# Performance work log

Hardware: AMD Instinct MI355X
Metric: run time of the kernel (lower is better)

Reference implementation:

```python
import jax, jax.numpy as jnp
import numpy as np

L = 16            # number of levels
F = 2             # features per level
T = 1 << 17       # hashmap size per level (power of 2)
N_TREES = 8       # forest blocks
N = 2_000_000     # query points
RES = np.array([16, 22, 30, 41, 55, 75, 102, 139, 188, 256, 348, 472, 642, 872, 1184, 1608], dtype=np.int64)
# 8 trilinear corner offsets [8,3]
OFFS = np.stack(np.meshgrid([0, 1], [0, 1], [0, 1], indexing='ij'), axis=-1).reshape(8, 3).astype(np.int32)
PRIMES = (np.uint32(1), np.uint32(2654435761), np.uint32(805459861))


def _hash(coords):
    # coords: [N,8,3] int32 grid corner coords -> [N,8] table index (NGP spatial hash)
    c = coords.astype(jnp.uint32)
    h = (c[..., 0] * PRIMES[0]) ^ (c[..., 1] * PRIMES[1]) ^ (c[..., 2] * PRIMES[2])
    return (h & jnp.uint32(T - 1)).astype(jnp.int32)


def setup_inputs() -> dict:
    key = jax.random.key(0)
    k1, k2, k3 = jax.random.split(key, 3)
    block_x = jax.random.uniform(k1, (N, 3), minval=-1.0, maxval=1.0, dtype=jnp.float32)
    bound = 1e-4
    params = jax.random.uniform(k2, (N_TREES, L, T, F), minval=-bound, maxval=bound, dtype=jnp.float32)
    block_inds = jax.random.randint(k3, (N,), 0, N_TREES)
    return {"block_x": block_x, "params": params, "block_inds": block_inds}


def reference(block_x, params, block_inds):
    # block_x in [-1,1]^3 -> [0,1]^3 (matches `block_x / 2.0 + 0.5` in forward)
    x01 = block_x * 0.5 + 0.5
    offs = jnp.asarray(OFFS)                    # [8,3]
    offs_b = jnp.asarray(OFFS, dtype=bool)      # [8,3]
    outs = []
    for l in range(L):
        R = int(RES[l])
        pos = x01 * (R - 1)                     # [N,3]
        p0 = jnp.floor(pos)
        w = pos - p0                            # trilinear fracs [N,3]
        p0i = p0.astype(jnp.int32)
        corners = jnp.clip(p0i[:, None, :] + offs[None], 0, R - 1)   # [N,8,3]
        idx = _hash(corners)                                          # [N,8]
        feats = params[block_inds[:, None], l, idx, :]                # [N,8,F] per-tree gather
        wc = jnp.prod(jnp.where(offs_b[None], w[:, None, :], 1.0 - w[:, None, :]), axis=-1)  # [N,8]
        outs.append(jnp.einsum('nc,ncf->nf', wc, feats))              # [N,F]
    return jnp.concatenate(outs, axis=-1)        # [N, L*F]
```

## Files before the change

### kernel.cpp

```cpp
#include <hip/hip_runtime.h>

#define NLEVELS 16
#define TSIZE 131072
#define TMASK (TSIZE - 1)
#define NBUCK 32768

typedef float f32x4 __attribute__((ext_vector_type(4)));

__device__ __constant__ float RM1_TAB[16] = {
    15.f, 21.f, 29.f, 40.f, 54.f, 74.f, 101.f, 138.f,
    187.f, 255.f, 347.f, 471.f, 641.f, 871.f, 1183.f, 1607.f
};

__device__ __forceinline__ unsigned spread4(unsigned v) {
    v = (v | (v << 4)) & 0x0C3u;
    v = (v | (v << 2)) & 0x249u;
    return v;
}

__device__ __forceinline__ unsigned bucket_key(float x, float y, float z, unsigned tree) {
    const int cx = min(max((int)((x * 0.5f + 0.5f) * 16.f), 0), 15);
    const int cy = min(max((int)((y * 0.5f + 0.5f) * 16.f), 0), 15);
    const int cz = min(max((int)((z * 0.5f + 0.5f) * 16.f), 0), 15);
    const unsigned m = spread4((unsigned)cx) | (spread4((unsigned)cy) << 1)
                     | (spread4((unsigned)cz) << 2);
    return (tree << 12) | m;
}


__global__ __launch_bounds__(256) void k_hist(const float* __restrict__ xs,
                                              const int* __restrict__ inds, int N,
                                              unsigned* __restrict__ hist) {
    const int i = blockIdx.x * 256 + threadIdx.x;
    if (i >= N) return;
    const unsigned key = bucket_key(xs[3 * i], xs[3 * i + 1], xs[3 * i + 2],
                                    (unsigned)(inds[i] & 7));
    atomicAdd(&hist[key], 1u);
}

__global__ __launch_bounds__(1024) void k_scan(const unsigned* __restrict__ hist,
                                               unsigned* __restrict__ cursor) {
    __shared__ unsigned sums[1024];
    const int t = threadIdx.x;
    const int per = NBUCK / 1024;
    unsigned s = 0;
    #pragma unroll
    for (int j = 0; j < per; ++j) s += hist[t * per + j];
    sums[t] = s;
    __syncthreads();
    for (int off = 1; off < 1024; off <<= 1) {
        const unsigned add = (t >= off) ? sums[t - off] : 0u;
        __syncthreads();
        sums[t] += add;
        __syncthreads();
    }
    unsigned run = (t == 0) ? 0u : sums[t - 1];
    #pragma unroll
    for (int j = 0; j < per; ++j) {
        cursor[t * per + j] = run;
        run += hist[t * per + j];
    }
}

__global__ __launch_bounds__(256) void k_scatter(const float* __restrict__ xs,
                                                 const int* __restrict__ inds, int N,
                                                 unsigned* __restrict__ cursor,
                                                 float4* __restrict__ sorted) {
    const int i = blockIdx.x * 256 + threadIdx.x;
    if (i >= N) return;
    const float x = xs[3 * i], y = xs[3 * i + 1], z = xs[3 * i + 2];
    const unsigned tree = (unsigned)(inds[i] & 7);
    const unsigned key = bucket_key(x, y, z, tree);
    const unsigned pos = atomicAdd(&cursor[key], 1u);
    sorted[pos] = make_float4(x, y, z, __uint_as_float(((unsigned)i) | (tree << 24)));
}


__device__ __forceinline__ void level_load(const float4 p, int tree, int l,
                                           const float* __restrict__ params,
                                           float2 f[8],
                                           float& wx, float& wy, float& wz) {
    const float rm1 = RM1_TAB[l];
    const int rmax = (int)rm1;

    const float px = (p.x * 0.5f + 0.5f) * rm1;
    const float py = (p.y * 0.5f + 0.5f) * rm1;
    const float pz = (p.z * 0.5f + 0.5f) * rm1;
    const float fx = floorf(px), fy = floorf(py), fz = floorf(pz);
    wx = px - fx; wy = py - fy; wz = pz - fz;
    const int ix = (int)fx, iy = (int)fy, iz = (int)fz;

    const int x0 = min(max(ix, 0), rmax), x1 = min(max(ix + 1, 0), rmax);
    const int y0 = min(max(iy, 0), rmax), y1 = min(max(iy + 1, 0), rmax);
    const int z0 = min(max(iz, 0), rmax), z1 = min(max(iz + 1, 0), rmax);

    const unsigned hx0 = (unsigned)x0;
    const unsigned hx1 = (unsigned)x1;
    const unsigned hy0 = (unsigned)y0 * 2654435761u;
    const unsigned hy1 = (unsigned)y1 * 2654435761u;
    const unsigned hz0 = (unsigned)z0 * 805459861u;
    const unsigned hz1 = (unsigned)z1 * 805459861u;

    const float2* __restrict__ tbl =
        (const float2*)(params + (size_t)(tree * NLEVELS + l) * (TSIZE * 2));

    const unsigned m00 = hy0 ^ hz0;
    const unsigned m01 = hy0 ^ hz1;
    const unsigned m10 = hy1 ^ hz0;
    const unsigned m11 = hy1 ^ hz1;
    const unsigned i000 = (hx0 ^ m00) & TMASK;
    const unsigned i001 = (hx0 ^ m01) & TMASK;
    const unsigned i010 = (hx0 ^ m10) & TMASK;
    const unsigned i011 = (hx0 ^ m11) & TMASK;

    const bool pairOK = ((x0 & 1) == 0) && (x1 == x0 + 1);
    if (pairOK) {
        const float4* __restrict__ tbl4 = (const float4*)tbl;
        const float4 q00 = tbl4[i000 >> 1];
        const float4 q01 = tbl4[i001 >> 1];
        const float4 q10 = tbl4[i010 >> 1];
        const float4 q11 = tbl4[i011 >> 1];
        f[0] = (i000 & 1) ? make_float2(q00.z, q00.w) : make_float2(q00.x, q00.y);
        f[4] = (i000 & 1) ? make_float2(q00.x, q00.y) : make_float2(q00.z, q00.w);
        f[1] = (i001 & 1) ? make_float2(q01.z, q01.w) : make_float2(q01.x, q01.y);
        f[5] = (i001 & 1) ? make_float2(q01.x, q01.y) : make_float2(q01.z, q01.w);
        f[2] = (i010 & 1) ? make_float2(q10.z, q10.w) : make_float2(q10.x, q10.y);
        f[6] = (i010 & 1) ? make_float2(q10.x, q10.y) : make_float2(q10.z, q10.w);
        f[3] = (i011 & 1) ? make_float2(q11.z, q11.w) : make_float2(q11.x, q11.y);
        f[7] = (i011 & 1) ? make_float2(q11.x, q11.y) : make_float2(q11.z, q11.w);
    } else {
        const unsigned i100 = (hx1 ^ m00) & TMASK;
        const unsigned i101 = (hx1 ^ m01) & TMASK;
        const unsigned i110 = (hx1 ^ m10) & TMASK;
        const unsigned i111 = (hx1 ^ m11) & TMASK;
        f[0] = tbl[i000]; f[1] = tbl[i001];
        f[2] = tbl[i010]; f[3] = tbl[i011];
        f[4] = tbl[i100]; f[5] = tbl[i101];
        f[6] = tbl[i110]; f[7] = tbl[i111];
    }
}

__device__ __forceinline__ float2 level_fma(const float2 f[8],
                                            float wx, float wy, float wz) {
    const float wx0 = 1.f - wx, wy0 = 1.f - wy, wz0 = 1.f - wz;
    const float w0 = wx0 * wy0 * wz0;
    const float w1 = wx0 * wy0 * wz;
    const float w2 = wx0 * wy  * wz0;
    const float w3 = wx0 * wy  * wz;
    const float w4 = wx  * wy0 * wz0;
    const float w5 = wx  * wy0 * wz;
    const float w6 = wx  * wy  * wz0;
    const float w7 = wx  * wy  * wz;
    float a0 = 0.f, a1 = 0.f;
    a0 = fmaf(w0, f[0].x, a0); a1 = fmaf(w0, f[0].y, a1);
    a0 = fmaf(w1, f[1].x, a0); a1 = fmaf(w1, f[1].y, a1);
    a0 = fmaf(w2, f[2].x, a0); a1 = fmaf(w2, f[2].y, a1);
    a0 = fmaf(w3, f[3].x, a0); a1 = fmaf(w3, f[3].y, a1);
    a0 = fmaf(w4, f[4].x, a0); a1 = fmaf(w4, f[4].y, a1);
    a0 = fmaf(w5, f[5].x, a0); a1 = fmaf(w5, f[5].y, a1);
    a0 = fmaf(w6, f[6].x, a0); a1 = fmaf(w6, f[6].y, a1);
    a0 = fmaf(w7, f[7].x, a0); a1 = fmaf(w7, f[7].y, a1);
    return make_float2(a0, a1);
}


__global__ __launch_bounds__(256) void k_main(const float4* __restrict__ sorted,
                                              const float* __restrict__ params,
                                              float4* __restrict__ out4,
                                              int N, int nc, int band_sz) {
    const int b = blockIdx.x;
    const int j = b & 7;
    const int chunk = b >> 3;
    const int band = chunk / band_sz;
    const int v = (j + band) & 7;
    const int i = chunk * 256 + threadIdx.x;
    if (i >= N) return;

    const float4 p = sorted[i];
    const unsigned wbits = __float_as_uint(p.w);
    const int n = (int)(wbits & 0xFFFFFFu);
    const int tree = (int)(wbits >> 24);

    float2 fA[8], fB[8];
    float wxA, wyA, wzA, wxB, wyB, wzB;

    level_load(p, tree, 2 * v,     params, fA, wxA, wyA, wzA);
    level_load(p, tree, 2 * v + 1, params, fB, wxB, wyB, wzB);

    const float2 rA = level_fma(fA, wxA, wyA, wzA);
    const float2 rB = level_fma(fB, wxB, wyB, wzB);

    out4[(size_t)n * 8 + v] = make_float4(rA.x, rA.y, rB.x, rB.y);
}


__global__ __launch_bounds__(256) void lotd_fwd_fused(
    const float* __restrict__ xs, const float* __restrict__ params,
    const int* __restrict__ inds, float* __restrict__ out, int N)
{
    const int g = blockIdx.x * 256 + threadIdx.x;
    const int n = g >> 4;
    if (n >= N) return;
    const int l = g & 15;
    const float rm1 = RM1_TAB[l];
    const int rmax = (int)rm1;
    const float x = xs[3 * n], y = xs[3 * n + 1], z = xs[3 * n + 2];
    const int tree = inds[n];
    const float px = (x * 0.5f + 0.5f) * rm1;
    const float py = (y * 0.5f + 0.5f) * rm1;
    const float pz = (z * 0.5f + 0.5f) * rm1;
    const float fx = floorf(px), fy = floorf(py), fz = floorf(pz);
    const float wx = px - fx, wy = py - fy, wz = pz - fz;
    const int ix = (int)fx, iy = (int)fy, iz = (int)fz;
    const int x0 = min(max(ix, 0), rmax), x1 = min(max(ix + 1, 0), rmax);
    const int y0 = min(max(iy, 0), rmax), y1 = min(max(iy + 1, 0), rmax);
    const int z0 = min(max(iz, 0), rmax), z1 = min(max(iz + 1, 0), rmax);
    const unsigned hx0 = (unsigned)x0, hx1 = (unsigned)x1;
    const unsigned hy0 = (unsigned)y0 * 2654435761u, hy1 = (unsigned)y1 * 2654435761u;
    const unsigned hz0 = (unsigned)z0 * 805459861u,  hz1 = (unsigned)z1 * 805459861u;
    const float2* tbl = (const float2*)(params + (size_t)(tree * NLEVELS + l) * (TSIZE * 2));
    const float2 f000 = tbl[(hx0 ^ hy0 ^ hz0) & TMASK];
    const float2 f001 = tbl[(hx0 ^ hy0 ^ hz1) & TMASK];
    const float2 f010 = tbl[(hx0 ^ hy1 ^ hz0) & TMASK];
    const float2 f011 = tbl[(hx0 ^ hy1 ^ hz1) & TMASK];
    const float2 f100 = tbl[(hx1 ^ hy0 ^ hz0) & TMASK];
    const float2 f101 = tbl[(hx1 ^ hy0 ^ hz1) & TMASK];
    const float2 f110 = tbl[(hx1 ^ hy1 ^ hz0) & TMASK];
    const float2 f111 = tbl[(hx1 ^ hy1 ^ hz1) & TMASK];
    const float wx0 = 1.f - wx, wy0 = 1.f - wy, wz0 = 1.f - wz;
    float a0 = 0.f, a1 = 0.f;
    a0 = fmaf(wx0*wy0*wz0, f000.x, a0); a1 = fmaf(wx0*wy0*wz0, f000.y, a1);
    a0 = fmaf(wx0*wy0*wz , f001.x, a0); a1 = fmaf(wx0*wy0*wz , f001.y, a1);
    a0 = fmaf(wx0*wy *wz0, f010.x, a0); a1 = fmaf(wx0*wy *wz0, f010.y, a1);
    a0 = fmaf(wx0*wy *wz , f011.x, a0); a1 = fmaf(wx0*wy *wz , f011.y, a1);
    a0 = fmaf(wx *wy0*wz0, f100.x, a0); a1 = fmaf(wx *wy0*wz0, f100.y, a1);
    a0 = fmaf(wx *wy0*wz , f101.x, a0); a1 = fmaf(wx *wy0*wz , f101.y, a1);
    a0 = fmaf(wx *wy *wz0, f110.x, a0); a1 = fmaf(wx *wy *wz0, f110.y, a1);
    a0 = fmaf(wx *wy *wz , f111.x, a0); a1 = fmaf(wx *wy *wz , f111.y, a1);
    ((float2*)out)[(size_t)n * 16 + l] = make_float2(a0, a1);
}

extern "C" void kernel_launch(void* const* d_in, const int* in_sizes, int n_in,
                              void* d_out, int out_size, void* d_ws, size_t ws_size,
                              hipStream_t stream) {
    const float* xs     = (const float*)d_in[0];
    const float* params = (const float*)d_in[1];
    const int*   inds   = (const int*)d_in[2];
    float*       out    = (float*)d_out;

    const int N = in_sizes[0] / 3;
    const int nc = (N + 255) / 256;
    const int band_sz = (nc + 7) / 8;

    const size_t hist_bytes   = (size_t)NBUCK * 4;
    const size_t head_bytes   = 2 * hist_bytes;
    const size_t sorted_bytes = ((size_t)N * 16 + 255) & ~(size_t)255;
    const size_t need = head_bytes + sorted_bytes;

    if (ws_size < need) {
        const int total = N * NLEVELS;
        lotd_fwd_fused<<<(total + 255) / 256, 256, 0, stream>>>(xs, params, inds, out, N);
        return;
    }

    unsigned* hist   = (unsigned*)d_ws;
    unsigned* cursor = (unsigned*)((char*)d_ws + hist_bytes);
    float4*   sorted = (float4*)((char*)d_ws + head_bytes);

    hipMemsetAsync(hist, 0, hist_bytes, stream);
    k_hist<<<nc, 256, 0, stream>>>(xs, inds, N, hist);
    k_scan<<<1, 1024, 0, stream>>>(hist, cursor);
    k_scatter<<<nc, 256, 0, stream>>>(xs, inds, N, cursor, sorted);

    k_main<<<nc * 8, 256, 0, stream>>>(sorted, params, (float4*)out, N, nc, band_sz);
}
```

Measured before the change: 854.9 us.

## Process all 16 levels per thread in one kernel instead of level-pair blocks

The main kernel now has each thread compute all 16 levels for its sorted point, launching nc blocks instead of nc*8. Block indices are remapped so each of the 8 interleaved groups covers a contiguous range of chunks. Each point's position and tree are read once and the full 128-byte output row is written by one thread, which cuts redundant sorted-point reads and spreads the output writes less. In exchange, the per-level banding that kept concurrent blocks on the same level's table slice is gone, so L2 locality for params may drop, and there is less parallelism plus higher register pressure under the 8-waves launch bound.

New measurement: 2.301 ms. +169.2%, slower.

```diff
diff --git a/kernel.cpp b/kernel.cpp
--- a/kernel.cpp
+++ b/kernel.cpp
@@ -164,16 +164,15 @@
 }
 
 
-__global__ __launch_bounds__(256) void k_main(const float4* __restrict__ sorted,
-                                              const float* __restrict__ params,
-                                              float4* __restrict__ out4,
-                                              int N, int nc, int band_sz) {
+__global__ __launch_bounds__(256, 8) void k_all(const float4* __restrict__ sorted,
+                                                const float* __restrict__ params,
+                                                float4* __restrict__ out4,
+                                                int N, int nc) {
     const int b = blockIdx.x;
+    const int q = nc >> 3, r = nc & 7;
     const int j = b & 7;
-    const int chunk = b >> 3;
-    const int band = chunk / band_sz;
-    const int v = (j + band) & 7;
-    const int i = chunk * 256 + threadIdx.x;
+    const int chunk = j * q + min(j, r) + (b >> 3);
+    const int i = chunk * 256 + (int)threadIdx.x;
     if (i >= N) return;
 
     const float4 p = sorted[i];
@@ -181,16 +180,22 @@
     const int n = (int)(wbits & 0xFFFFFFu);
     const int tree = (int)(wbits >> 24);
 
-    float2 fA[8], fB[8];
-    float wxA, wyA, wzA, wxB, wyB, wzB;
-
-    level_load(p, tree, 2 * v,     params, fA, wxA, wyA, wzA);
-    level_load(p, tree, 2 * v + 1, params, fB, wxB, wyB, wzB);
-
-    const float2 rA = level_fma(fA, wxA, wyA, wzA);
-    const float2 rB = level_fma(fB, wxB, wyB, wzB);
-
-    out4[(size_t)n * 8 + v] = make_float4(rA.x, rA.y, rB.x, rB.y);
+    #pragma unroll
+    for (int h = 0; h < 2; ++h) {
+        float2 row[8];
+        #pragma unroll
+        for (int l = 0; l < 8; ++l) {
+            float2 f[8]; float wx, wy, wz;
+            level_load(p, tree, 8 * h + l, params, f, wx, wy, wz);
+            row[l] = level_fma(f, wx, wy, wz);
+        }
+        #pragma unroll
+        for (int k = 0; k < 4; ++k) {
+            out4[(size_t)n * 8 + 4 * h + k] =
+                make_float4(row[2 * k].x, row[2 * k].y,
+                            row[2 * k + 1].x, row[2 * k + 1].y);
+        }
+    }
 }
 
 
@@ -250,7 +255,6 @@
 
     const int N = in_sizes[0] / 3;
     const int nc = (N + 255) / 256;
-    const int band_sz = (nc + 7) / 8;
 
     const size_t hist_bytes   = (size_t)NBUCK * 4;
     const size_t head_bytes   = 2 * hist_bytes;
@@ -272,5 +276,5 @@
     k_scan<<<1, 1024, 0, stream>>>(hist, cursor);
     k_scatter<<<nc, 256, 0, stream>>>(xs, inds, N, cursor, sorted);
 
-    k_main<<<nc * 8, 256, 0, stream>>>(sorted, params, (float4*)out, N, nc, band_sz);
-}
+    k_all<<<nc, 256, 0, stream>>>(sorted, params, (float4*)out, N, nc);
+}
```
